# Kernel optimization log

Measured on AMD Instinct MI355X. Metric: run time of the kernel, lower is better.

The kernel has to match this reference:

```python
import jax, jax.numpy as jnp
import numpy as np

N_NODES = 100000
N_EDGES = 1600000
IN_DIM = 192   # n_shapes(64) * n_dims(3)
H1, H2 = 64, 32


def _glorot(key, shape):
    lim = np.sqrt(6.0 / (shape[0] + shape[1])).astype(np.float32)
    return jax.random.uniform(key, shape, jnp.float32, -lim, lim)


def setup_inputs() -> dict:
    key = jax.random.key(0)
    ks = jax.random.split(key, 8)
    verts = jax.random.normal(ks[0], (N_NODES, IN_DIM), jnp.float32)
    edges = jax.random.randint(ks[1], (N_EDGES, 2), 0, N_NODES)
    return {
        "verts": verts,
        "edges": edges,
        "W0_1": _glorot(ks[2], (IN_DIM, H1)),
        "W1_1": _glorot(ks[3], (IN_DIM, H1)),
        "b1": jnp.zeros((H1,), jnp.float32),
        "W0_2": _glorot(ks[4], (H1, H2)),
        "W1_2": _glorot(ks[5], (H1, H2)),
        "b2": jnp.zeros((H2,), jnp.float32),
    }


def cheb_conv(x, src, dst, W0, W1, b, n):
    # ChebConv K=2 with lambda_max=2: L_hat = -D^{-1/2} A D^{-1/2} (zero diagonal)
    deg = jax.ops.segment_sum(jnp.ones(src.shape, x.dtype), src, num_segments=n)
    d_inv = jnp.where(deg > 0, jax.lax.rsqrt(jnp.maximum(deg, 1.0)), 0.0)
    norm = -d_inv[src] * d_inv[dst]                      # [E]
    Tx1 = jax.ops.segment_sum(norm[:, None] * x[src], dst, num_segments=n)  # [n,F]
    return x @ W0 + Tx1 @ W1 + b


def reference(verts, edges, W0_1, W1_1, b1, W0_2, W1_2, b2):
    n = verts.shape[0]
    src, dst = edges[:, 0], edges[:, 1]  # edge_index rows after edges.t()
    x = jax.nn.relu(cheb_conv(verts, src, dst, W0_1, W1_1, b1, n))
    return cheb_conv(x, src, dst, W0_2, W1_2, b2, n)
```

## Files before the change

### kernel.cpp

```cpp
#include <hip/hip_runtime.h>

#define N_NODES 100000
#define N_EDGES 1600000
#define IN_DIM  192
#define H1      64
#define H2      32
#define NBKT    391
#define CAP_D   4608
#define K1GRID  2345

typedef __attribute__((ext_vector_type(8))) short short8;
typedef __attribute__((ext_vector_type(4))) float f32x4;

__device__ inline short f2bf(float f) {
    union { float f; unsigned u; } v; v.f = f;
    unsigned r = (v.u + 0x7FFFu + ((v.u >> 16) & 1u)) >> 16;
    return (short)r;
}
__device__ inline float bf2f(unsigned short s) {
    union { unsigned u; float f; } v; v.u = ((unsigned)s) << 16;
    return v.f;
}

__global__ __launch_bounds__(256) void prep_w_kernel(
    const float* __restrict__ W0_1, const float* __restrict__ W1_1,
    const float* __restrict__ W0_2, const float* __restrict__ W1_2,
    short* __restrict__ Bt1, short* __restrict__ Bt2, int* __restrict__ bucket_next) {
    if (blockIdx.x == 0) {
        for (int i = threadIdx.x; i < 1024; i += 256)
            bucket_next[i] = (i & 511) * CAP_D;
    }
    int idx = blockIdx.x * 256 + threadIdx.x;
    if (idx < 128 * IN_DIM) {
        int n = idx / IN_DIM, k = idx % IN_DIM;
        float v = (n < H1) ? W0_1[(size_t)k * H1 + n] : W1_1[(size_t)k * H1 + (n - H1)];
        Bt1[idx] = f2bf(v);
    } else {
        int j = idx - 128 * IN_DIM;
        if (j < 64 * H1) {
            int n = j / H1, k = j % H1;
            float v = (n < H2) ? W0_2[(size_t)k * H2 + n] : W1_2[(size_t)k * H2 + (n - H2)];
            Bt2[j] = f2bf(v);
        }
    }
}

__global__ __launch_bounds__(256) void k1_fused(
    const int* __restrict__ edges, int* __restrict__ bucket_next,
    int* __restrict__ bins_dst, unsigned char* __restrict__ bins_src,
    const float* __restrict__ verts, const short* __restrict__ Bt1,
    const float* __restrict__ b1, short* __restrict__ hbase, short* __restrict__ y1b) {
    __shared__ int cntd[512];
    __shared__ int curd[512];
    __shared__ int cnts[512];
    __shared__ int curs[512];
    int b = blockIdx.x;
    int tid = threadIdx.x;
    if (b % 3 == 0) {
        int p = b / 3;
        cntd[tid] = 0; cntd[tid + 256] = 0;
        cnts[tid] = 0; cnts[tid + 256] = 0;
        __syncthreads();
        int ebase = p * 2048 + tid * 8;
        int2 ed[8]; int bd[8], bs[8];
        if (ebase + 7 < N_EDGES) {
            const int4* e4 = (const int4*)edges;
            int i4 = ebase >> 1;
#pragma unroll
            for (int i = 0; i < 4; ++i) {
                int4 q = e4[i4 + i];
                ed[2 * i]     = make_int2(q.x, q.y);
                ed[2 * i + 1] = make_int2(q.z, q.w);
            }
#pragma unroll
            for (int i = 0; i < 8; ++i) {
                bd[i] = ed[i].y >> 8;
                bs[i] = ed[i].x >> 8;
                atomicAdd(&cntd[bd[i]], 1);
                atomicAdd(&cnts[bs[i]], 1);
            }
        } else {
#pragma unroll
            for (int i = 0; i < 8; ++i) {
                int e = ebase + i;
                if (e < N_EDGES) {
                    ed[i] = ((const int2*)edges)[e];
                    bd[i] = ed[i].y >> 8;
                    bs[i] = ed[i].x >> 8;
                    atomicAdd(&cntd[bd[i]], 1);
                    atomicAdd(&cnts[bs[i]], 1);
                } else { bd[i] = -1; bs[i] = -1; }
            }
        }
        __syncthreads();
        {
            int c;
            c = cntd[tid];       curd[tid]       = (c > 0) ? atomicAdd(&bucket_next[tid], c) : 0;
            c = cntd[tid + 256]; curd[tid + 256] = (c > 0) ? atomicAdd(&bucket_next[tid + 256], c) : 0;
            c = cnts[tid];       curs[tid]       = (c > 0) ? atomicAdd(&bucket_next[512 + tid], c) : 0;
            c = cnts[tid + 256]; curs[tid + 256] = (c > 0) ? atomicAdd(&bucket_next[512 + tid + 256], c) : 0;
        }
        __syncthreads();
#pragma unroll
        for (int i = 0; i < 8; ++i) {
            if (bd[i] >= 0) {
                int sd = atomicAdd(&curd[bd[i]], 1);
                if (sd < (bd[i] + 1) * CAP_D)
                    bins_dst[sd] = ((ed[i].y & 255) << 17) | ed[i].x;
                int ss = atomicAdd(&curs[bs[i]], 1);
                if (ss < (bs[i] + 1) * CAP_D)
                    bins_src[ss] = (unsigned char)(ed[i].x & 255);
            }
        }
        return;
    }
    int g = b - b / 3 - 1;
    int lane = tid & 63;
    int wave = tid >> 6;
    int rowbase = g * 64 + wave * 16;
    int lr = lane & 15;
    int lk = (lane >> 4) * 8;

    int row = rowbase + lr;
    int rc = (row < N_NODES) ? row : (N_NODES - 1);
    const float* p = verts + (size_t)rc * IN_DIM + lk;
    short8 a[6];
#pragma unroll
    for (int ks = 0; ks < 6; ++ks) {
        f32x4 u0 = *(const f32x4*)(p + ks * 32);
        f32x4 u1 = *(const f32x4*)(p + ks * 32 + 4);
        short8 t;
        t[0] = f2bf(u0[0]); t[1] = f2bf(u0[1]); t[2] = f2bf(u0[2]); t[3] = f2bf(u0[3]);
        t[4] = f2bf(u1[0]); t[5] = f2bf(u1[1]); t[6] = f2bf(u1[2]); t[7] = f2bf(u1[3]);
        a[ks] = t;
    }

    f32x4 acc[8] = {};
#pragma unroll
    for (int cf = 0; cf < 8; ++cf) {
        const short* bp = Bt1 + (size_t)(cf * 16 + lr) * IN_DIM + lk;
#pragma unroll
        for (int ks = 0; ks < 6; ++ks) {
            short8 bb = *(const short8*)(bp + ks * 32);
            acc[cf] = __builtin_amdgcn_mfma_f32_16x16x32_bf16(a[ks], bb, acc[cf], 0, 0, 0);
        }
    }

    int srow = (lane >> 4) * 4;
#pragma unroll
    for (int cf = 0; cf < 8; ++cf) {
        int colc = cf * 16 + lr;
        float bias = (colc < H1) ? b1[colc] : 0.f;
#pragma unroll
        for (int r = 0; r < 4; ++r) {
            int orow = rowbase + srow + r;
            if (orow < N_NODES) {
                float v = acc[cf][r];
                if (colc < H1) hbase[(size_t)orow * H1 + colc] = f2bf(v + bias);
                else           y1b[(size_t)orow * H1 + (colc - H1)] = f2bf(v);
            }
        }
    }
}

__global__ __launch_bounds__(256) void csr_kernel(
    const int* __restrict__ bins_dst, const unsigned char* __restrict__ bins_src,
    const int* __restrict__ bucket_next, float* __restrict__ dinv,
    int* __restrict__ row_beg, int* __restrict__ row_end, int* __restrict__ col,
    const unsigned short* __restrict__ y1b, short* __restrict__ y1s) {
    __shared__ int cnt_l[256];
    __shared__ int seg_l[256];
    __shared__ int s[256];
    __shared__ int dcnt[256];
    __shared__ float dinv_l[256];
    int b = blockIdx.x;
    int tid = threadIdx.x;
    int beg = b * CAP_D;
    int filld = bucket_next[b] - beg;
    if (filld > CAP_D) filld = CAP_D;
    int fills = bucket_next[512 + b] - beg;
    if (fills > CAP_D) fills = CAP_D;
    cnt_l[tid] = 0;
    dcnt[tid] = 0;
    __syncthreads();
    for (int i = tid; i < filld; i += 256)
        atomicAdd(&cnt_l[bins_dst[beg + i] >> 17], 1);
    for (int i = tid; i < fills; i += 256)
        atomicAdd(&dcnt[bins_src[beg + i]], 1);
    __syncthreads();
    int v = cnt_l[tid];
    s[tid] = v;
    __syncthreads();
    for (int off = 1; off < 256; off <<= 1) {
        int t = (tid >= off) ? s[tid - off] : 0;
        __syncthreads();
        s[tid] += t;
        __syncthreads();
    }
    int excl = s[tid] - v;
    seg_l[tid] = beg + excl;
    int n = b * 256 + tid;
    int d = dcnt[tid];
    float dv = (d > 0) ? rsqrtf((float)d) : 0.f;
    dinv_l[tid] = dv;
    if (n < N_NODES) {
        row_beg[n] = beg + excl;
        row_end[n] = beg + excl + v;
        dinv[n] = dv;
    }
    __syncthreads();
    for (int i = tid; i < filld; i += 256) {
        int w = bins_dst[beg + i];
        int slot = atomicAdd(&seg_l[w >> 17], 1);
        col[slot] = w & 0x1FFFF;
    }
    int nb = b * 256;
    int nmax = N_NODES - nb; if (nmax > 256) nmax = 256;
    for (int idx = tid; idx < nmax * 8; idx += 256) {
        int r = idx >> 3, j = idx & 7;
        float w = dinv_l[r];
        size_t off = (size_t)(nb + r) * H1 + j * 8;
        short8 vv = *(const short8*)&y1b[off];
        short8 o;
#pragma unroll
        for (int q = 0; q < 8; ++q) o[q] = f2bf(w * bf2f((unsigned short)vv[q]));
        *(short8*)&y1s[off] = o;
    }
}

__global__ __launch_bounds__(512) void g1g2_kernel(
    const int* __restrict__ row_beg, const int* __restrict__ row_end,
    const int* __restrict__ col, const float* __restrict__ dinv,
    const unsigned short* __restrict__ hbase, const unsigned short* __restrict__ y1s,
    const short* __restrict__ Bt2, const float* __restrict__ b2,
    float* __restrict__ out, short* __restrict__ y2s) {
    __shared__ short hb_l[16][68];
    int tid = threadIdx.x, lane = tid & 63, wv = tid >> 6;
    int nb = blockIdx.x * 16;
    for (int j = 0; j < 2; ++j) {
        int n = nb + wv * 2 + j;
        int beg = row_beg[n], end = row_end[n];
        float acc = 0.f;
        int i = beg;
        for (; i + 8 <= end; i += 8) {
            int s0 = col[i], s1 = col[i + 1], s2 = col[i + 2], s3 = col[i + 3];
            int s4 = col[i + 4], s5 = col[i + 5], s6 = col[i + 6], s7 = col[i + 7];
            float v0 = bf2f(y1s[(size_t)s0 * H1 + lane]);
            float v1 = bf2f(y1s[(size_t)s1 * H1 + lane]);
            float v2 = bf2f(y1s[(size_t)s2 * H1 + lane]);
            float v3 = bf2f(y1s[(size_t)s3 * H1 + lane]);
            float v4 = bf2f(y1s[(size_t)s4 * H1 + lane]);
            float v5 = bf2f(y1s[(size_t)s5 * H1 + lane]);
            float v6 = bf2f(y1s[(size_t)s6 * H1 + lane]);
            float v7 = bf2f(y1s[(size_t)s7 * H1 + lane]);
            acc += ((v0 + v1) + (v2 + v3)) + ((v4 + v5) + (v6 + v7));
        }
        for (; i + 4 <= end; i += 4) {
            int s0 = col[i], s1 = col[i + 1], s2 = col[i + 2], s3 = col[i + 3];
            float v0 = bf2f(y1s[(size_t)s0 * H1 + lane]);
            float v1 = bf2f(y1s[(size_t)s1 * H1 + lane]);
            float v2 = bf2f(y1s[(size_t)s2 * H1 + lane]);
            float v3 = bf2f(y1s[(size_t)s3 * H1 + lane]);
            acc += (v0 + v1) + (v2 + v3);
        }
        for (; i < end; ++i)
            acc += bf2f(y1s[(size_t)col[i] * H1 + lane]);
        float hf = bf2f(hbase[(size_t)n * H1 + lane]) - dinv[n] * acc;
        hb_l[wv * 2 + j][lane] = f2bf(fmaxf(hf, 0.f));
    }
    __syncthreads();
    if (wv < 4) {
        int lr = lane & 15;
        int lk = (lane >> 4) * 8;
        short8 a0 = *(const short8*)&hb_l[lr][lk];
        short8 a1 = *(const short8*)&hb_l[lr][32 + lk];
        const short* bp = Bt2 + (size_t)(wv * 16 + lr) * H1 + lk;
        short8 b0 = *(const short8*)(bp);
        short8 b1 = *(const short8*)(bp + 32);
        f32x4 acc2 = {};
        acc2 = __builtin_amdgcn_mfma_f32_16x16x32_bf16(a0, b0, acc2, 0, 0, 0);
        acc2 = __builtin_amdgcn_mfma_f32_16x16x32_bf16(a1, b1, acc2, 0, 0, 0);
        int srow = (lane >> 4) * 4;
        int colc = wv * 16 + lr;
        float bias = (colc < H2) ? b2[colc] : 0.f;
#pragma unroll
        for (int r = 0; r < 4; ++r) {
            int n = nb + srow + r;
            float v = acc2[r];
            if (colc < H2) out[(size_t)n * H2 + colc] = v + bias;
            else           y2s[(size_t)n * H2 + (colc - H2)] = f2bf(dinv[n] * v);
        }
    }
}

__global__ __launch_bounds__(256) void gather2_kernel(
    const int* __restrict__ row_beg, const int* __restrict__ row_end,
    const int* __restrict__ col, const float* __restrict__ dinv,
    const unsigned short* __restrict__ y2s, float* __restrict__ out) {
    int wave = (blockIdx.x * 256 + threadIdx.x) >> 6;
    int lane = threadIdx.x & 63;
    int n = wave * 2 + (lane >> 5);
    if (n >= N_NODES) return;
    int c32 = lane & 31;
    int beg = row_beg[n], end = row_end[n];
    float acc = 0.f;
    int i = beg;
    for (; i + 8 <= end; i += 8) {
        int s0 = col[i], s1 = col[i + 1], s2 = col[i + 2], s3 = col[i + 3];
        int s4 = col[i + 4], s5 = col[i + 5], s6 = col[i + 6], s7 = col[i + 7];
        float v0 = bf2f(y2s[(size_t)s0 * H2 + c32]);
        float v1 = bf2f(y2s[(size_t)s1 * H2 + c32]);
        float v2 = bf2f(y2s[(size_t)s2 * H2 + c32]);
        float v3 = bf2f(y2s[(size_t)s3 * H2 + c32]);
        float v4 = bf2f(y2s[(size_t)s4 * H2 + c32]);
        float v5 = bf2f(y2s[(size_t)s5 * H2 + c32]);
        float v6 = bf2f(y2s[(size_t)s6 * H2 + c32]);
        float v7 = bf2f(y2s[(size_t)s7 * H2 + c32]);
        acc += ((v0 + v1) + (v2 + v3)) + ((v4 + v5) + (v6 + v7));
    }
    for (; i + 4 <= end; i += 4) {
        int s0 = col[i], s1 = col[i + 1], s2 = col[i + 2], s3 = col[i + 3];
        float v0 = bf2f(y2s[(size_t)s0 * H2 + c32]);
        float v1 = bf2f(y2s[(size_t)s1 * H2 + c32]);
        float v2 = bf2f(y2s[(size_t)s2 * H2 + c32]);
        float v3 = bf2f(y2s[(size_t)s3 * H2 + c32]);
        acc += (v0 + v1) + (v2 + v3);
    }
    for (; i < end; ++i)
        acc += bf2f(y2s[(size_t)col[i] * H2 + c32]);
    size_t idx = (size_t)n * H2 + c32;
    out[idx] = out[idx] - dinv[n] * acc;
}

extern "C" void kernel_launch(void* const* d_in, const int* in_sizes, int n_in,
                              void* d_out, int out_size, void* d_ws, size_t ws_size,
                              hipStream_t stream) {
    const float* verts = (const float*)d_in[0];
    const int*   edges = (const int*)  d_in[1];
    const float* W0_1  = (const float*)d_in[2];
    const float* W1_1  = (const float*)d_in[3];
    const float* b1    = (const float*)d_in[4];
    const float* W0_2  = (const float*)d_in[5];
    const float* W1_2  = (const float*)d_in[6];
    const float* b2    = (const float*)d_in[7];
    float* out = (float*)d_out;

    char* ws = (char*)d_ws;
    auto align256 = [](size_t x) { return (x + 255) & ~(size_t)255; };
    size_t o = 0;
    auto alloc = [&](size_t bytes) { size_t r = o; o = align256(o + bytes); return r; };

    int*   bucket_next = (int*)  (ws + alloc((size_t)1024 * 4));
    int*   bins_dst    = (int*)  (ws + alloc((size_t)NBKT * CAP_D * 4));
    unsigned char* bins_src = (unsigned char*)(ws + alloc((size_t)NBKT * CAP_D));
    int*   col         = (int*)  (ws + alloc((size_t)NBKT * CAP_D * 4));
    int*   row_beg     = (int*)  (ws + alloc((size_t)N_NODES * 4));
    int*   row_end     = (int*)  (ws + alloc((size_t)N_NODES * 4));
    float* dinv        = (float*)(ws + alloc((size_t)N_NODES * 4));
    short* Bt1         = (short*)(ws + alloc((size_t)128 * IN_DIM * 2));
    short* Bt2         = (short*)(ws + alloc((size_t)64 * H1 * 2));
    short* hbase       = (short*)(ws + alloc((size_t)N_NODES * H1 * 2));
    short* y1b         = (short*)(ws + alloc((size_t)N_NODES * H1 * 2));
    short* y1s         = (short*)(ws + alloc((size_t)N_NODES * H1 * 2));
    short* y2s         = (short*)(ws + alloc((size_t)N_NODES * H2 * 2));

    prep_w_kernel<<<112, 256, 0, stream>>>(W0_1, W1_1, W0_2, W1_2, Bt1, Bt2, bucket_next);

    k1_fused  <<<K1GRID, 256, 0, stream>>>(edges, bucket_next, bins_dst, bins_src,
                                           verts, Bt1, b1, hbase, y1b);
    csr_kernel<<<NBKT, 256, 0, stream>>>(bins_dst, bins_src, bucket_next, dinv,
                                         row_beg, row_end, col,
                                         (const unsigned short*)y1b, y1s);

    g1g2_kernel<<<N_NODES / 16, 512, 0, stream>>>(row_beg, row_end, col, dinv,
                                                  (const unsigned short*)hbase,
                                                  (const unsigned short*)y1s,
                                                  Bt2, b2, out, y2s);
    gather2_kernel<<<(N_NODES + 7) / 8, 256, 0, stream>>>(row_beg, row_end, col, dinv,
                                                          (const unsigned short*)y2s, out);
}
```

Baseline: 201.2 us.

## Partition bucket counters per XCC and halve g1g2 block size

Each bucket's global fill counters are split into eight sub-ranges, one per XCC, chosen from the hardware XCC_ID register. This keeps global atomics from different dies apart and avoids cross-die atomic contention while binning edges. The CSR kernel then walks the eight sub-ranges per bucket. Separately, g1g2 now runs with 256 threads, each wave gathering 4 nodes instead of 2, and all four waves take part in the MFMA stage. Each sub-range holds at most 640 entries, so a skewed bucket/XCC split could overflow and silently drop edges, which is a correctness risk.

Measured after the change: 201.4 us. Within noise of the previous version (+0.1%).

```diff
diff --git a/kernel.cpp b/kernel.cpp
--- a/kernel.cpp
+++ b/kernel.cpp
@@ -6,7 +6,8 @@
 #define H1      64
 #define H2      32
 #define NBKT    391
-#define CAP_D   4608
+#define SUB     640
+#define CAP_D   5120
 #define K1GRID  2345
 
 typedef __attribute__((ext_vector_type(8))) short short8;
@@ -20,6 +21,11 @@
 __device__ inline float bf2f(unsigned short s) {
     union { unsigned u; float f; } v; v.u = ((unsigned)s) << 16;
     return v.f;
+}
+__device__ inline int get_xcc() {
+    int x;
+    asm volatile("s_getreg_b32 %0, hwreg(HW_REG_XCC_ID)" : "=s"(x));
+    return x & 7;
 }
 
 __global__ __launch_bounds__(256) void prep_w_kernel(
@@ -27,8 +33,10 @@
     const float* __restrict__ W0_2, const float* __restrict__ W1_2,
     short* __restrict__ Bt1, short* __restrict__ Bt2, int* __restrict__ bucket_next) {
     if (blockIdx.x == 0) {
-        for (int i = threadIdx.x; i < 1024; i += 256)
-            bucket_next[i] = (i & 511) * CAP_D;
+        for (int i = threadIdx.x; i < 8192; i += 256) {
+            int xcc = i >> 10, b = i & 511;
+            bucket_next[i] = b * CAP_D + xcc * SUB;
+        }
     }
     int idx = blockIdx.x * 256 + threadIdx.x;
     if (idx < 128 * IN_DIM) {
@@ -58,6 +66,8 @@
     int tid = threadIdx.x;
     if (b % 3 == 0) {
         int p = b / 3;
+        int xcc = get_xcc();
+        int subend = xcc * SUB + SUB;
         cntd[tid] = 0; cntd[tid + 256] = 0;
         cnts[tid] = 0; cnts[tid + 256] = 0;
         __syncthreads();
@@ -94,21 +104,23 @@
         }
         __syncthreads();
         {
+            int* bn_d = bucket_next + xcc * 1024;
+            int* bn_s = bn_d + 512;
             int c;
-            c = cntd[tid];       curd[tid]       = (c > 0) ? atomicAdd(&bucket_next[tid], c) : 0;
-            c = cntd[tid + 256]; curd[tid + 256] = (c > 0) ? atomicAdd(&bucket_next[tid + 256], c) : 0;
-            c = cnts[tid];       curs[tid]       = (c > 0) ? atomicAdd(&bucket_next[512 + tid], c) : 0;
-            c = cnts[tid + 256]; curs[tid + 256] = (c > 0) ? atomicAdd(&bucket_next[512 + tid + 256], c) : 0;
+            c = cntd[tid];       curd[tid]       = (c > 0) ? atomicAdd(&bn_d[tid], c) : 0;
+            c = cntd[tid + 256]; curd[tid + 256] = (c > 0) ? atomicAdd(&bn_d[tid + 256], c) : 0;
+            c = cnts[tid];       curs[tid]       = (c > 0) ? atomicAdd(&bn_s[tid], c) : 0;
+            c = cnts[tid + 256]; curs[tid + 256] = (c > 0) ? atomicAdd(&bn_s[tid + 256], c) : 0;
         }
         __syncthreads();
 #pragma unroll
         for (int i = 0; i < 8; ++i) {
             if (bd[i] >= 0) {
                 int sd = atomicAdd(&curd[bd[i]], 1);
-                if (sd < (bd[i] + 1) * CAP_D)
+                if (sd < bd[i] * CAP_D + subend)
                     bins_dst[sd] = ((ed[i].y & 255) << 17) | ed[i].x;
                 int ss = atomicAdd(&curs[bs[i]], 1);
-                if (ss < (bs[i] + 1) * CAP_D)
+                if (ss < bs[i] * CAP_D + subend)
                     bins_src[ss] = (unsigned char)(ed[i].x & 255);
             }
         }
@@ -176,17 +188,20 @@
     int b = blockIdx.x;
     int tid = threadIdx.x;
     int beg = b * CAP_D;
-    int filld = bucket_next[b] - beg;
-    if (filld > CAP_D) filld = CAP_D;
-    int fills = bucket_next[512 + b] - beg;
-    if (fills > CAP_D) fills = CAP_D;
     cnt_l[tid] = 0;
     dcnt[tid] = 0;
     __syncthreads();
-    for (int i = tid; i < filld; i += 256)
-        atomicAdd(&cnt_l[bins_dst[beg + i] >> 17], 1);
-    for (int i = tid; i < fills; i += 256)
-        atomicAdd(&dcnt[bins_src[beg + i]], 1);
+    for (int x = 0; x < 8; ++x) {
+        int sbeg = beg + x * SUB;
+        int fd = bucket_next[x * 1024 + b] - sbeg;
+        if (fd > SUB) fd = SUB;
+        for (int i = tid; i < fd; i += 256)
+            atomicAdd(&cnt_l[bins_dst[sbeg + i] >> 17], 1);
+        int fs = bucket_next[x * 1024 + 512 + b] - sbeg;
+        if (fs > SUB) fs = SUB;
+        for (int i = tid; i < fs; i += 256)
+            atomicAdd(&dcnt[bins_src[sbeg + i]], 1);
+    }
     __syncthreads();
     int v = cnt_l[tid];
     s[tid] = v;
@@ -209,10 +224,15 @@
         dinv[n] = dv;
     }
     __syncthreads();
-    for (int i = tid; i < filld; i += 256) {
-        int w = bins_dst[beg + i];
-        int slot = atomicAdd(&seg_l[w >> 17], 1);
-        col[slot] = w & 0x1FFFF;
+    for (int x = 0; x < 8; ++x) {
+        int sbeg = beg + x * SUB;
+        int fd = bucket_next[x * 1024 + b] - sbeg;
+        if (fd > SUB) fd = SUB;
+        for (int i = tid; i < fd; i += 256) {
+            int w = bins_dst[sbeg + i];
+            int slot = atomicAdd(&seg_l[w >> 17], 1);
+            col[slot] = w & 0x1FFFF;
+        }
     }
     int nb = b * 256;
     int nmax = N_NODES - nb; if (nmax > 256) nmax = 256;
@@ -228,7 +248,7 @@
     }
 }
 
-__global__ __launch_bounds__(512) void g1g2_kernel(
+__global__ __launch_bounds__(256) void g1g2_kernel(
     const int* __restrict__ row_beg, const int* __restrict__ row_end,
     const int* __restrict__ col, const float* __restrict__ dinv,
     const unsigned short* __restrict__ hbase, const unsigned short* __restrict__ y1s,
@@ -237,8 +257,8 @@
     __shared__ short hb_l[16][68];
     int tid = threadIdx.x, lane = tid & 63, wv = tid >> 6;
     int nb = blockIdx.x * 16;
-    for (int j = 0; j < 2; ++j) {
-        int n = nb + wv * 2 + j;
+    for (int j = 0; j < 4; ++j) {
+        int n = nb + wv * 4 + j;
         int beg = row_beg[n], end = row_end[n];
         float acc = 0.f;
         int i = beg;
@@ -266,30 +286,28 @@
         for (; i < end; ++i)
             acc += bf2f(y1s[(size_t)col[i] * H1 + lane]);
         float hf = bf2f(hbase[(size_t)n * H1 + lane]) - dinv[n] * acc;
-        hb_l[wv * 2 + j][lane] = f2bf(fmaxf(hf, 0.f));
-    }
-    __syncthreads();
-    if (wv < 4) {
-        int lr = lane & 15;
-        int lk = (lane >> 4) * 8;
-        short8 a0 = *(const short8*)&hb_l[lr][lk];
-        short8 a1 = *(const short8*)&hb_l[lr][32 + lk];
-        const short* bp = Bt2 + (size_t)(wv * 16 + lr) * H1 + lk;
-        short8 b0 = *(const short8*)(bp);
-        short8 b1 = *(const short8*)(bp + 32);
-        f32x4 acc2 = {};
-        acc2 = __builtin_amdgcn_mfma_f32_16x16x32_bf16(a0, b0, acc2, 0, 0, 0);
-        acc2 = __builtin_amdgcn_mfma_f32_16x16x32_bf16(a1, b1, acc2, 0, 0, 0);
-        int srow = (lane >> 4) * 4;
-        int colc = wv * 16 + lr;
-        float bias = (colc < H2) ? b2[colc] : 0.f;
-#pragma unroll
-        for (int r = 0; r < 4; ++r) {
-            int n = nb + srow + r;
-            float v = acc2[r];
-            if (colc < H2) out[(size_t)n * H2 + colc] = v + bias;
-            else           y2s[(size_t)n * H2 + (colc - H2)] = f2bf(dinv[n] * v);
-        }
+        hb_l[wv * 4 + j][lane] = f2bf(fmaxf(hf, 0.f));
+    }
+    __syncthreads();
+    int lr = lane & 15;
+    int lk = (lane >> 4) * 8;
+    short8 a0 = *(const short8*)&hb_l[lr][lk];
+    short8 a1 = *(const short8*)&hb_l[lr][32 + lk];
+    const short* bp = Bt2 + (size_t)(wv * 16 + lr) * H1 + lk;
+    short8 b0 = *(const short8*)(bp);
+    short8 b1 = *(const short8*)(bp + 32);
+    f32x4 acc2 = {};
+    acc2 = __builtin_amdgcn_mfma_f32_16x16x32_bf16(a0, b0, acc2, 0, 0, 0);
+    acc2 = __builtin_amdgcn_mfma_f32_16x16x32_bf16(a1, b1, acc2, 0, 0, 0);
+    int srow = (lane >> 4) * 4;
+    int colc = wv * 16 + lr;
+    float bias = (colc < H2) ? b2[colc] : 0.f;
+#pragma unroll
+    for (int r = 0; r < 4; ++r) {
+        int n = nb + srow + r;
+        float v = acc2[r];
+        if (colc < H2) out[(size_t)n * H2 + colc] = v + bias;
+        else           y2s[(size_t)n * H2 + (colc - H2)] = f2bf(dinv[n] * v);
     }
 }
 
@@ -350,7 +368,7 @@
     size_t o = 0;
     auto alloc = [&](size_t bytes) { size_t r = o; o = align256(o + bytes); return r; };
 
-    int*   bucket_next = (int*)  (ws + alloc((size_t)1024 * 4));
+    int*   bucket_next = (int*)  (ws + alloc((size_t)8192 * 4));
     int*   bins_dst    = (int*)  (ws + alloc((size_t)NBKT * CAP_D * 4));
     unsigned char* bins_src = (unsigned char*)(ws + alloc((size_t)NBKT * CAP_D));
     int*   col         = (int*)  (ws + alloc((size_t)NBKT * CAP_D * 4));
@@ -372,7 +390,7 @@
                                          row_beg, row_end, col,
                                          (const unsigned short*)y1b, y1s);
 
-    g1g2_kernel<<<N_NODES / 16, 512, 0, stream>>>(row_beg, row_end, col, dinv,
+    g1g2_kernel<<<N_NODES / 16, 256, 0, stream>>>(row_beg, row_end, col, dinv,
                                                   (const unsigned short*)hbase,
                                                   (const unsigned short*)y1s,
                                                   Bt2, b2, out, y2s);
```
